# Optimization experiments

Measured on AMD Instinct MI355X. Metric: run time of the kernel, lower is better.

Reference implementation:

```python
import jax, jax.numpy as jnp
import numpy as np

L, B, D, N = 4096, 8, 1024, 16


def setup_inputs() -> dict:
    key = jax.random.key(0)
    ks = jax.random.split(key, 6)
    # ema_expansion_matrix init: alternating +-1 plus small noise (per reset_parameters)
    sign = jnp.where(jnp.arange(N) % 2 == 1, -1.0, 1.0)[None, :, None]
    return {
        "x": jax.random.normal(ks[0], (L, B, D), dtype=jnp.float32),
        "damping_factor": 0.2 * jax.random.normal(ks[1], (D, N, 1), dtype=jnp.float32),
        "decay_factor": 0.2 * jax.random.normal(ks[2], (D, N, 1), dtype=jnp.float32),
        "ema_expansion_matrix": sign + 0.02 * jax.random.normal(ks[3], (D, N, 1), dtype=jnp.float32),
        "kernel_projection_matrix": jax.random.normal(ks[4], (D, N), dtype=jnp.float32),
        "residual_weight": jax.random.normal(ks[5], (D,), dtype=jnp.float32),
    }


def reference(x, damping_factor, decay_factor, ema_expansion_matrix,
              kernel_projection_matrix, residual_weight):
    # x: (L, B, D)
    length = x.shape[0]
    num_heads = damping_factor.shape[1]
    scaling = (1.0 / num_heads) ** 0.5

    residual = x * residual_weight  # (L, B, D)
    xc = jnp.transpose(x, (1, 2, 0))  # (B, D, L)

    # EMA coefficients
    p = jax.nn.sigmoid(damping_factor)                     # (D, N, 1)
    q = 1.0 - p * jax.nn.sigmoid(decay_factor)             # (D, N, 1)

    # Vandermonde kernel: (D, N, L) -> project to (D, L)
    t = jnp.arange(length, dtype=x.dtype)[None, None, :]
    kernel_dnl = p * ema_expansion_matrix * jnp.exp(t * jnp.log(q))
    kernel = jnp.einsum('dnl,dn->dl', kernel_dnl, kernel_projection_matrix * scaling)

    # Causal FFT convolution with n = 2L
    n_fft = 2 * length
    k_f = jnp.fft.rfft(kernel, n=n_fft)                    # (D, n/2+1)
    x_f = jnp.fft.rfft(xc, n=n_fft)                        # (B, D, n/2+1)
    out = jnp.fft.irfft(x_f * k_f, n=n_fft)[..., :length]  # (B, D, L)

    out = jnp.transpose(out, (2, 0, 1)) + residual         # (L, B, D)
    return jax.nn.relu(out)
```

## Files before the change

### kernel.cpp

```cpp
#include <hip/hip_runtime.h>
#include <math.h>

#define L 4096
#define B 8
#define D 1024
#define NH 16
#define COUT 256
#define WB 128
#define NCHUNK (L / COUT)
#define BD 8192
#define DBLK 128
#define TL 16
#define NBUF 4

#define REP4(F) F(0) F(1) F(2) F(3)

typedef float f2 __attribute__((ext_vector_type(2)));

__device__ __forceinline__ float sigmoidf(float v) {
    return 1.0f / (1.0f + __expf(-v));
}

#define UPD(i) s##i = __builtin_elementwise_fma(q##i, s##i, xv2);
#define UPDALL UPD(0) UPD(1) UPD(2) UPD(3)
#define ACC(i) s##i = __builtin_elementwise_fma(q##i, s##i, xv2); \
               y2 = __builtin_elementwise_fma(P##i, s##i, y2);
#define ACCALL ACC(0) ACC(1) ACC(2) ACC(3)

#define GLD16(g, l) __builtin_amdgcn_global_load_lds( \
    (const __attribute__((address_space(1))) unsigned int*)(g), \
    (__attribute__((address_space(3))) unsigned int*)(l), 16, 0, 0)

#define VM(n) asm volatile("s_waitcnt vmcnt(" #n ")" ::: "memory")
#define MEMFENCE asm volatile("" ::: "memory")

__global__ void __launch_bounds__(256, 4)
ema_fused(const float* __restrict__ x,
          const float* __restrict__ damp,
          const float* __restrict__ decay,
          const float* __restrict__ ema,
          const float* __restrict__ proj,
          const float* __restrict__ rw,
          float* __restrict__ out) {
    const int tid  = threadIdx.x;
    const int lane = tid & 63;
    const int wv   = tid >> 6;
    const int h    = lane & 1;
    const int dloc = (wv << 5) + (lane >> 1);
    const int d    = blockIdx.x * DBLK + dloc;
    const int c    = blockIdx.y;
    const int b    = blockIdx.z;

    __shared__ float lds[NBUF][TL * DBLK];

    const float* dp = damp  + d * NH + h * 8;
    const float* dc = decay + d * NH + h * 8;
    const float* de = ema   + d * NH + h * 8;
    const float* pj = proj  + d * NH + h * 8;

#define DECLQS(i) f2 q##i, s##i;
    REP4(DECLQS)
#define INITQS(i) { \
        q##i.x = 1.0f - sigmoidf(dp[2*(i)])   * sigmoidf(dc[2*(i)]); \
        q##i.y = 1.0f - sigmoidf(dp[2*(i)+1]) * sigmoidf(dc[2*(i)+1]); \
        s##i.x = 0.0f; s##i.y = 0.0f; }
    REP4(INITQS)
#define DECLP(i) f2 P##i;
    REP4(DECLP)
#define INITP(i) { \
        P##i.x = sigmoidf(dp[2*(i)])   * de[2*(i)]   * pj[2*(i)]   * 0.25f; \
        P##i.y = sigmoidf(dp[2*(i)+1]) * de[2*(i)+1] * pj[2*(i)+1] * 0.25f; }
    REP4(INITP)
    const float weff = (h == 0) ? rw[d] : 0.0f;

    VM(0); MEMFENCE;

    const int wb = (c > 0) ? WB : 0;
    const int wt = wb / TL;
    const int nt = wt + COUT / TL;

    const float* xb = x + (size_t)(c * COUT - wb) * BD + (size_t)b * D
                        + (size_t)blockIdx.x * DBLK;
    const float* gsrc = xb + (size_t)((wv << 2) + (lane >> 5)) * BD
                           + ((lane & 31) << 2);

#define GLD(t) { \
        const float* g_ = gsrc + (size_t)(t) * (TL * BD); \
        float* l_ = &lds[(t) & 3][(wv << 2) * DBLK]; \
        GLD16(g_, l_); \
        GLD16(g_ + 2 * (size_t)BD, l_ + 2 * DBLK); }

    GLD(0) GLD(1) GLD(2)
    MEMFENCE;

    if (c > 0) {
        for (int t = 0; t < WB / TL; ++t) {
            VM(4);
            __builtin_amdgcn_s_barrier();
            MEMFENCE;
            GLD(t + 3)
            MEMFENCE;
            const float* bp = &lds[t & 3][dloc];
#pragma unroll
            for (int sl = 0; sl < TL; ++sl) {
                float xv = bp[sl * DBLK];
                f2 xv2; xv2.x = xv; xv2.y = xv;
                UPDALL
            }
        }
    }

    float* opb = out + (size_t)(c * COUT) * BD + (size_t)b * D + d;

#define OTILE(r, KWAIT, DOGLD) { \
        KWAIT; \
        __builtin_amdgcn_s_barrier(); \
        MEMFENCE; \
        if (DOGLD) GLD(wt + (r) + 3) \
        MEMFENCE; \
        const float* bp = &lds[(wt + (r)) & 3][dloc]; \
        float* op = opb + (size_t)(r) * (TL * BD); \
        _Pragma("unroll") \
        for (int sl = 0; sl < TL; ++sl) { \
            float xv = bp[sl * DBLK]; \
            f2 xv2; xv2.x = xv; xv2.y = xv; \
            f2 y2;  y2.x = xv * weff; y2.y = 0.0f; \
            ACCALL \
            float y = y2.x + y2.y; \
            y += __shfl_xor(y, 1); \
            op[(size_t)sl * BD] = fmaxf(y, 0.0f); \
        } }

    OTILE(0,  VM(4),  1)
    OTILE(1,  VM(20), 1)
    OTILE(2,  VM(36), 1)
#pragma unroll
    for (int r = 3; r <= 12; ++r) { OTILE(r, VM(52), 1) }
    OTILE(13, VM(52), 0)
    OTILE(14, VM(50), 0)
    OTILE(15, VM(48), 0)
}

extern "C" void kernel_launch(void* const* d_in, const int* in_sizes, int n_in,
                              void* d_out, int out_size, void* d_ws, size_t ws_size,
                              hipStream_t stream) {
    const float* x     = (const float*)d_in[0];
    const float* damp  = (const float*)d_in[1];
    const float* decay = (const float*)d_in[2];
    const float* ema   = (const float*)d_in[3];
    const float* proj  = (const float*)d_in[4];
    const float* rw    = (const float*)d_in[5];
    float* out = (float*)d_out;

    dim3 grid(D / DBLK, NCHUNK, B);
    ema_fused<<<grid, 256, 0, stream>>>(x, damp, decay, ema, proj, rw, out);
}
```

Baseline: 265.5 us.

## Map one channel per thread with 512-thread blocks and smaller time tiles

Each thread now runs all 16 EMA states for one channel instead of splitting them across a lane pair. This removes the per-output cross-lane shuffle, and split accumulators shorten the dependency chain. Blocks grow to 512 threads covering 512 channels, and time tiles shrink to 8 rows with the wait counts retuned to match. The cost is more registers per thread, lower occupancy from launch bounds (512,1), and a grid with only 2 blocks along the channel axis, so there are fewer blocks overall.

```diff
diff --git a/kernel.cpp b/kernel.cpp
--- a/kernel.cpp
+++ b/kernel.cpp
@@ -9,11 +9,11 @@
 #define WB 128
 #define NCHUNK (L / COUT)
 #define BD 8192
-#define DBLK 128
-#define TL 16
+#define DBLK 512
+#define TL 8
 #define NBUF 4
 
-#define REP4(F) F(0) F(1) F(2) F(3)
+#define REP8(F) F(0) F(1) F(2) F(3) F(4) F(5) F(6) F(7)
 
 typedef float f2 __attribute__((ext_vector_type(2)));
 
@@ -22,10 +22,12 @@
 }
 
 #define UPD(i) s##i = __builtin_elementwise_fma(q##i, s##i, xv2);
-#define UPDALL UPD(0) UPD(1) UPD(2) UPD(3)
-#define ACC(i) s##i = __builtin_elementwise_fma(q##i, s##i, xv2); \
-               y2 = __builtin_elementwise_fma(P##i, s##i, y2);
-#define ACCALL ACC(0) ACC(1) ACC(2) ACC(3)
+#define UPDALL UPD(0) UPD(1) UPD(2) UPD(3) UPD(4) UPD(5) UPD(6) UPD(7)
+#define ACCA(i) s##i = __builtin_elementwise_fma(q##i, s##i, xv2); \
+                yA = __builtin_elementwise_fma(P##i, s##i, yA);
+#define ACCB(i) s##i = __builtin_elementwise_fma(q##i, s##i, xv2); \
+                yB = __builtin_elementwise_fma(P##i, s##i, yB);
+#define ACCALL ACCA(0) ACCB(1) ACCA(2) ACCB(3) ACCA(4) ACCB(5) ACCA(6) ACCB(7)
 
 #define GLD16(g, l) __builtin_amdgcn_global_load_lds( \
     (const __attribute__((address_space(1))) unsigned int*)(g), \
@@ -34,7 +36,7 @@
 #define VM(n) asm volatile("s_waitcnt vmcnt(" #n ")" ::: "memory")
 #define MEMFENCE asm volatile("" ::: "memory")
 
-__global__ void __launch_bounds__(256, 4)
+__global__ void __launch_bounds__(512, 1)
 ema_fused(const float* __restrict__ x,
           const float* __restrict__ damp,
           const float* __restrict__ decay,
@@ -45,33 +47,32 @@
     const int tid  = threadIdx.x;
     const int lane = tid & 63;
     const int wv   = tid >> 6;
-    const int h    = lane & 1;
-    const int dloc = (wv << 5) + (lane >> 1);
-    const int d    = blockIdx.x * DBLK + dloc;
+    const int bx   = blockIdx.x;
     const int c    = blockIdx.y;
     const int b    = blockIdx.z;
+    const int d    = bx * DBLK + tid;
 
-    __shared__ float lds[NBUF][TL * DBLK];
+    __shared__ float lds[NBUF][TL][DBLK];
 
-    const float* dp = damp  + d * NH + h * 8;
-    const float* dc = decay + d * NH + h * 8;
-    const float* de = ema   + d * NH + h * 8;
-    const float* pj = proj  + d * NH + h * 8;
+    const float* dp = damp  + d * NH;
+    const float* dc = decay + d * NH;
+    const float* de = ema   + d * NH;
+    const float* pj = proj  + d * NH;
 
 #define DECLQS(i) f2 q##i, s##i;
-    REP4(DECLQS)
+    REP8(DECLQS)
 #define INITQS(i) { \
         q##i.x = 1.0f - sigmoidf(dp[2*(i)])   * sigmoidf(dc[2*(i)]); \
         q##i.y = 1.0f - sigmoidf(dp[2*(i)+1]) * sigmoidf(dc[2*(i)+1]); \
         s##i.x = 0.0f; s##i.y = 0.0f; }
-    REP4(INITQS)
+    REP8(INITQS)
 #define DECLP(i) f2 P##i;
-    REP4(DECLP)
+    REP8(DECLP)
 #define INITP(i) { \
         P##i.x = sigmoidf(dp[2*(i)])   * de[2*(i)]   * pj[2*(i)]   * 0.25f; \
         P##i.y = sigmoidf(dp[2*(i)+1]) * de[2*(i)+1] * pj[2*(i)+1] * 0.25f; }
-    REP4(INITP)
-    const float weff = (h == 0) ? rw[d] : 0.0f;
+    REP8(INITP)
+    const float w = rw[d];
 
     VM(0); MEMFENCE;
 
@@ -80,15 +81,13 @@
     const int nt = wt + COUT / TL;
 
     const float* xb = x + (size_t)(c * COUT - wb) * BD + (size_t)b * D
-                        + (size_t)blockIdx.x * DBLK;
-    const float* gsrc = xb + (size_t)((wv << 2) + (lane >> 5)) * BD
-                           + ((lane & 31) << 2);
+                        + (size_t)bx * DBLK;
 
 #define GLD(t) { \
-        const float* g_ = gsrc + (size_t)(t) * (TL * BD); \
-        float* l_ = &lds[(t) & 3][(wv << 2) * DBLK]; \
-        GLD16(g_, l_); \
-        GLD16(g_ + 2 * (size_t)BD, l_ + 2 * DBLK); }
+        const float* g_ = xb + (size_t)((t) * TL + wv) * BD + (lane << 2); \
+        float* l_ = &lds[(t) & 3][wv][0]; \
+        GLD16(g_,       l_); \
+        GLD16(g_ + 256, l_ + 256); }
 
     GLD(0) GLD(1) GLD(2)
     MEMFENCE;
@@ -100,7 +99,7 @@
             MEMFENCE;
             GLD(t + 3)
             MEMFENCE;
-            const float* bp = &lds[t & 3][dloc];
+            const float* bp = &lds[t & 3][0][tid];
 #pragma unroll
             for (int sl = 0; sl < TL; ++sl) {
                 float xv = bp[sl * DBLK];
@@ -110,7 +109,8 @@
         }
     }
 
-    float* opb = out + (size_t)(c * COUT) * BD + (size_t)b * D + d;
+    float* opb = out + (size_t)(c * COUT) * BD + (size_t)b * D
+                     + (size_t)bx * DBLK + tid;
 
 #define OTILE(r, KWAIT, DOGLD) { \
         KWAIT; \
@@ -118,27 +118,28 @@
         MEMFENCE; \
         if (DOGLD) GLD(wt + (r) + 3) \
         MEMFENCE; \
-        const float* bp = &lds[(wt + (r)) & 3][dloc]; \
+        const float* bp = &lds[(wt + (r)) & 3][0][tid]; \
         float* op = opb + (size_t)(r) * (TL * BD); \
         _Pragma("unroll") \
         for (int sl = 0; sl < TL; ++sl) { \
             float xv = bp[sl * DBLK]; \
             f2 xv2; xv2.x = xv; xv2.y = xv; \
-            f2 y2;  y2.x = xv * weff; y2.y = 0.0f; \
+            f2 yA;  yA.x = xv * w; yA.y = 0.0f; \
+            f2 yB;  yB.x = 0.0f;  yB.y = 0.0f; \
             ACCALL \
-            float y = y2.x + y2.y; \
-            y += __shfl_xor(y, 1); \
+            f2 yt = yA + yB; \
+            float y = yt.x + yt.y; \
             op[(size_t)sl * BD] = fmaxf(y, 0.0f); \
         } }
 
-    OTILE(0,  VM(4),  1)
-    OTILE(1,  VM(20), 1)
-    OTILE(2,  VM(36), 1)
+    OTILE(0, VM(4),  1)
+    OTILE(1, VM(12), 1)
+    OTILE(2, VM(20), 1)
 #pragma unroll
-    for (int r = 3; r <= 12; ++r) { OTILE(r, VM(52), 1) }
-    OTILE(13, VM(52), 0)
-    OTILE(14, VM(50), 0)
-    OTILE(15, VM(48), 0)
+    for (int r = 3; r <= 28; ++r) { OTILE(r, VM(28), 1) }
+    OTILE(29, VM(28), 0)
+    OTILE(30, VM(26), 0)
+    OTILE(31, VM(24), 0)
 }
 
 extern "C" void kernel_launch(void* const* d_in, const int* in_sizes, int n_in,
@@ -153,5 +154,5 @@
     float* out = (float*)d_out;
 
     dim3 grid(D / DBLK, NCHUNK, B);
-    ema_fused<<<grid, 256, 0, stream>>>(x, damp, decay, ema, proj, rw, out);
+    ema_fused<<<grid, 512, 0, stream>>>(x, damp, decay, ema, proj, rw, out);
 }
```

Result: faster. 250.1 us (-5.8%).
